# Optimization experiments

Measured on AMD Instinct MI355X. Metric: run time of the kernel, lower is better.

The kernel has to match this reference:

```python
import jax, jax.numpy as jnp
import numpy as np

NUM_ENT = 10000
NUM_REL = 230
S_DIM = 96
T_DIM = 32
DIM = S_DIM + T_DIM  # 128
N = 32768   # neighbors
Q = 4096    # unique query entities
E = 32768   # pooling edges
B = 1024    # batch triples
BN_EPS = 1e-5


def setup_inputs() -> dict:
    key = jax.random.key(0)
    ks = jax.random.split(key, 32)
    inp = {}
    inp["neighbor_idx"] = jax.random.randint(ks[0], (N,), 0, NUM_ENT)
    inp["rel_id"] = jax.random.randint(ks[1], (N,), 0, 2 * NUM_REL)
    inp["years"] = jax.random.uniform(ks[2], (N, 1), jnp.float32)
    inp["months"] = jax.random.uniform(ks[3], (N, 1), jnp.float32)
    inp["days"] = jax.random.uniform(ks[4], (N, 1), jnp.float32)
    inp["pool_src"] = jax.random.randint(ks[5], (E,), 0, N)
    inp["pool_dst"] = jax.random.randint(ks[6], (E,), 0, Q)
    inp["head_pos"] = jax.random.randint(ks[7], (B,), 0, Q)
    inp["tail_pos"] = jax.random.randint(ks[8], (B,), 0, Q)
    inp["rels"] = jax.random.randint(ks[9], (B,), 0, NUM_REL)
    # parameters (xavier-ish scales)
    inp["ent_embs"] = jax.random.normal(ks[10], (NUM_ENT, S_DIM), jnp.float32) * 0.05
    names = ["y_freq", "y_phi", "y_amp", "m_freq", "m_phi", "m_amp", "d_freq", "d_phi", "d_amp"]
    for i, n in enumerate(names):
        inp[n] = jax.random.normal(ks[11 + i], (NUM_ENT, T_DIM), jnp.float32) * 0.05
    inp["rel_embs"] = jax.random.normal(ks[20], (NUM_REL, DIM), jnp.float32) * 0.05
    inp["W"] = jax.random.normal(ks[21], (2 * NUM_REL, DIM, DIM), jnp.float32) * (1.0 / np.sqrt(DIM))
    inp["b"] = jnp.zeros((2 * NUM_REL, DIM), jnp.float32)
    inp["gamma"] = jnp.ones((2 * NUM_REL, DIM), jnp.float32)
    inp["beta"] = jnp.zeros((2 * NUM_REL, DIM), jnp.float32)
    return inp


def _forward(ent_embs, y_freq, y_phi, y_amp, m_freq, m_phi, m_amp,
             d_freq, d_phi, d_amp, rel_embs, W, b, gamma, beta,
             years, months, days,
             neighbor_idx, rel_id, pool_src, pool_dst, head_pos, tail_pos, rels):
    # diachronic time embedding: amp * sin(freq * t + phi), summed over y/m/d
    ty = y_amp[neighbor_idx] * jnp.sin(y_freq[neighbor_idx] * years + y_phi[neighbor_idx])
    tm = m_amp[neighbor_idx] * jnp.sin(m_freq[neighbor_idx] * months + m_phi[neighbor_idx])
    td = d_amp[neighbor_idx] * jnp.sin(d_freq[neighbor_idx] * days + d_phi[neighbor_idx])
    x = jnp.concatenate([ent_embs[neighbor_idx], ty + tm + td], axis=1)  # [N, DIM]

    # per-relation Linear (gather weights per neighbor)
    z = jnp.einsum('nd,nde->ne', x, W[rel_id]) + b[rel_id]  # [N, DIM]

    # per-relation-bucket BatchNorm (training stats, biased var); skipped for singleton buckets
    R2 = 2 * NUM_REL
    cnt = jax.ops.segment_sum(jnp.ones((z.shape[0],), z.dtype), rel_id, num_segments=R2)
    denom = jnp.maximum(cnt, 1.0)[:, None]
    mean = jax.ops.segment_sum(z, rel_id, num_segments=R2) / denom
    var = jax.ops.segment_sum(z * z, rel_id, num_segments=R2) / denom - mean * mean
    var = jnp.maximum(var, 0.0)
    zn = (z - mean[rel_id]) * jax.lax.rsqrt(var[rel_id] + BN_EPS) * gamma[rel_id] + beta[rel_id]
    z = jnp.where((cnt[rel_id] > 1.0)[:, None], zn, z)
    z = jax.nn.relu(z)

    # average pooling of neighbor features per query entity (PoolingLayer 'avg')
    psum = jax.ops.segment_sum(z[pool_src], pool_dst, num_segments=Q)
    pcnt = jax.ops.segment_sum(jnp.ones((pool_src.shape[0],), z.dtype), pool_dst, num_segments=Q)
    emb = psum / jnp.maximum(pcnt, 1.0)[:, None]  # [Q, DIM]

    # TransE-style scoring: -||h + r - t||_2 (dropout p=0 / eval mode)
    diff = emb[head_pos] + rel_embs[rels] - emb[tail_pos]
    return -jnp.sqrt(jnp.sum(diff * diff, axis=1))


def reference(neighbor_idx, rel_id, years, months, days, pool_src, pool_dst,
              head_pos, tail_pos, rels, ent_embs, y_freq, y_phi, y_amp,
              m_freq, m_phi, m_amp, d_freq, d_phi, d_amp, rel_embs, W, b, gamma, beta):
    return _forward(ent_embs, y_freq, y_phi, y_amp, m_freq, m_phi, m_amp,
                    d_freq, d_phi, d_amp, rel_embs, W, b, gamma, beta,
                    years, months, days,
                    neighbor_idx, rel_id, pool_src, pool_dst, head_pos, tail_pos, rels)
```

## Files before the change

### kernel.cpp

```cpp
#include <hip/hip_runtime.h>
#include <math.h>

#define NUM_ENT 10000
#define NUM_REL 230
#define R2      460
#define S_DIM   96
#define T_DIM   32
#define DIM     128
#define N_NBR   32768
#define Q_ENT   4096
#define E_EDGE  32768
#define B_TRI   1024
#define BN_EPS  1e-5f
#define CHUNK   64

typedef __attribute__((ext_vector_type(8))) short bf16x8;
typedef __attribute__((ext_vector_type(4))) float f32x4;

__device__ __forceinline__ unsigned short f2bf(float f) {
    unsigned int u = __float_as_uint(f);
    u = (u + 0x7FFFu + ((u >> 16) & 1u)) >> 16;
    return (unsigned short)u;
}
__device__ __forceinline__ float bf2f(unsigned short us) {
    return __uint_as_float((unsigned int)us << 16);
}

__device__ __forceinline__ int XIDX(int m, int d) {
    return (m * DIM + d) ^ ((m & 7) << 3);
}

__global__ void k_zero(int* __restrict__ p, int n4) {
    int i = blockIdx.x * blockDim.x + threadIdx.x;
    if (i < n4) ((int4*)p)[i] = make_int4(0, 0, 0, 0);
}

__global__ __launch_bounds__(256, 2) void k_front(
    const float* __restrict__ W, unsigned short* __restrict__ Wfrag,
    const int* __restrict__ rel, const int* __restrict__ pdst,
    int* __restrict__ hist_rel, int* __restrict__ hist_dst)
{
    const int t = threadIdx.x;
    if (blockIdx.x >= R2) {
        const int i = (blockIdx.x - R2) * 256 + t;
        if (i < N_NBR) atomicAdd(&hist_rel[rel[i]], 1);
        if (i < E_EDGE) atomicAdd(&hist_dst[pdst[i]], 1);
        return;
    }
    const int r = blockIdx.x;
    __shared__ float Wl[DIM * DIM];
    {
        const float4* Wg = (const float4*)(W + (size_t)r * DIM * DIM);
        float4* Wl4 = (float4*)Wl;
        #pragma unroll
        for (int i = 0; i < 16; ++i)
            Wl4[t + i * 256] = Wg[t + i * 256];
    }
    __syncthreads();
    unsigned short* dst = Wfrag + (size_t)r * DIM * DIM;
    #pragma unroll
    for (int it = 0; it < 8; ++it) {
        const int id = t + it * 256;
        const int lane = id & 63;
        const int h    = (id >> 6) & 1;
        const int wv   = (id >> 7) & 3;
        const int kk   = (id >> 9) & 3;
        const int n  = 32 * wv + 16 * h + (lane & 15);
        const int kb = 32 * kk + 8 * (lane >> 4);
        ushort4 lo, hi;
        lo.x = f2bf(Wl[(kb + 0) * DIM + n]);
        lo.y = f2bf(Wl[(kb + 1) * DIM + n]);
        lo.z = f2bf(Wl[(kb + 2) * DIM + n]);
        lo.w = f2bf(Wl[(kb + 3) * DIM + n]);
        hi.x = f2bf(Wl[(kb + 4) * DIM + n]);
        hi.y = f2bf(Wl[(kb + 5) * DIM + n]);
        hi.z = f2bf(Wl[(kb + 6) * DIM + n]);
        hi.w = f2bf(Wl[(kb + 7) * DIM + n]);
        *(ushort4*)&dst[id * 8]     = lo;
        *(ushort4*)&dst[id * 8 + 4] = hi;
    }
}

__global__ void k_scan_both(const int* __restrict__ hist_rel, int* __restrict__ offsets,
                            int* __restrict__ cur_rel,
                            const int* __restrict__ hist_dst, int* __restrict__ dst_off,
                            int* __restrict__ cur_dst)
{
    __shared__ int s[1024];
    const int t = threadIdx.x;
    if (blockIdx.x == 0) {
        const int h = (t < R2) ? hist_rel[t] : 0;
        if (t < 512) s[t] = h;
        __syncthreads();
        for (int off = 1; off < 512; off <<= 1) {
            int a = (t >= off && t < 512) ? s[t - off] : 0;
            __syncthreads();
            if (t < 512) s[t] += a;
            __syncthreads();
        }
        if (t == 0) offsets[0] = 0;
        if (t < R2) {
            offsets[t + 1] = s[t];
            cur_rel[t] = s[t] - h;
        }
    } else {
        const int base = t * 4;
        int v0 = hist_dst[base], v1 = hist_dst[base + 1];
        int v2 = hist_dst[base + 2], v3 = hist_dst[base + 3];
        s[t] = v0 + v1 + v2 + v3;
        __syncthreads();
        for (int off = 1; off < 1024; off <<= 1) {
            int a = (t >= off) ? s[t - off] : 0;
            __syncthreads();
            s[t] += a;
            __syncthreads();
        }
        int run = (t > 0) ? s[t - 1] : 0;
        dst_off[base] = run; cur_dst[base] = run; run += v0;
        dst_off[base + 1] = run; cur_dst[base + 1] = run; run += v1;
        dst_off[base + 2] = run; cur_dst[base + 2] = run; run += v2;
        dst_off[base + 3] = run; cur_dst[base + 3] = run; run += v3;
        if (t == 1023) dst_off[4096] = run;
    }
}

__global__ void k_scatter(const int* __restrict__ rel,
                          int* __restrict__ cur_rel, int* __restrict__ order,
                          int* __restrict__ rankpack,
                          const int* __restrict__ psrc, const int* __restrict__ pdst,
                          int* __restrict__ cur_dst, int* __restrict__ eorder_src) {
    int i = blockIdx.x * blockDim.x + threadIdx.x;
    if (i < N_NBR) {
        const int r = rel[i];
        const int pos = atomicAdd(&cur_rel[r], 1);
        order[pos] = i;
        rankpack[i] = pos | (r << 17);
    }
    if (i < E_EDGE) {
        eorder_src[atomicAdd(&cur_dst[pdst[i]], 1)] = psrc[i];
    }
}

__global__ __launch_bounds__(512, 4) void k_matvec(
    const int* __restrict__ order, const int* __restrict__ offsets,
    const int* __restrict__ nbr,
    const float* __restrict__ years, const float* __restrict__ months, const float* __restrict__ days,
    const float* __restrict__ ent,
    const float* __restrict__ yf, const float* __restrict__ yp, const float* __restrict__ ya,
    const float* __restrict__ mf, const float* __restrict__ mp, const float* __restrict__ ma,
    const float* __restrict__ df, const float* __restrict__ dp, const float* __restrict__ da,
    const unsigned short* __restrict__ Wfrag, const float* __restrict__ bias,
    const float* __restrict__ gamma, const float* __restrict__ beta,
    unsigned short* __restrict__ z_s, float2* __restrict__ scsh)
{
    const int r     = blockIdx.x;
    const int start = offsets[r];
    const int cnt   = offsets[r + 1] - start;

    __shared__ __align__(16) unsigned short Xl[2][CHUNK * DIM];
    __shared__ int s_ord[2][CHUNK];
    __shared__ int s_ni[2][CHUNK];
    __shared__ float bnred[8][2][16][2];

    const int t    = threadIdx.x;
    const int wid  = t >> 6;
    const int half = wid >> 2;
    const int wv   = wid & 3;
    const int lane = t & 63;
    const int l15  = lane & 15;
    const int g    = lane >> 4;

    const int nn0 = 32 * wv + l15;
    const int nn1 = nn0 + 16;
    const float bv0 = bias[r * DIM + nn0];
    const float bv1 = bias[r * DIM + nn1];

    float lsum0 = 0.f, lsq0 = 0.f, lsum1 = 0.f, lsq1 = 0.f;
    const unsigned short* Wr = Wfrag + (size_t)r * DIM * DIM;

    for (int cbase = 0; cbase < cnt; cbase += 2 * CHUNK) {
        const int hbase = cbase + half * CHUNK;
        const int mcnt  = min(CHUNK, max(0, cnt - hbase));

        if (t < 2 * CHUNK) {
            const int hh = t >> 6;
            const int m  = t & 63;
            const int gb = cbase + hh * CHUNK;
            int o = -1, ni = 0;
            if (gb + m < cnt) { o = order[start + gb + m]; ni = nbr[o]; }
            s_ord[hh][m] = o;
            s_ni[hh][m]  = ni;
        }
        __syncthreads();

        if (mcnt > 0) {
            const int lt = t & 255;
            const int m = lt >> 2, s = lt & 3;
            const int ni = s_ni[half][m];
            const bool vm = (m < mcnt);
            #pragma unroll
            for (int kk = 0; kk < 6; ++kk) {
                const int d = 4 * (s + 4 * kk);
                float4 e = *(const float4*)(ent + (size_t)ni * S_DIM + d);
                ushort4 b;
                b.x = vm ? f2bf(e.x) : 0; b.y = vm ? f2bf(e.y) : 0;
                b.z = vm ? f2bf(e.z) : 0; b.w = vm ? f2bf(e.w) : 0;
                *(ushort4*)&Xl[half][XIDX(m, d)] = b;
            }
            const int o = s_ord[half][m] < 0 ? 0 : s_ord[half][m];
            const float yr = years[o], mo = months[o], dy = days[o];
            #pragma unroll
            for (int hh = 0; hh < 2; ++hh) {
                const int j0 = s * 8 + hh * 4;
                const size_t tb = (size_t)ni * T_DIM + j0;
                const float4 vyf = *(const float4*)(yf + tb), vyp = *(const float4*)(yp + tb), vya = *(const float4*)(ya + tb);
                const float4 vmf = *(const float4*)(mf + tb), vmp = *(const float4*)(mp + tb), vma = *(const float4*)(ma + tb);
                const float4 vdf = *(const float4*)(df + tb), vdp = *(const float4*)(dp + tb), vda = *(const float4*)(da + tb);
                ushort4 b;
                #pragma unroll
                for (int j = 0; j < 4; ++j) {
                    const float fy = ((const float*)&vyf)[j] * yr + ((const float*)&vyp)[j];
                    const float fm = ((const float*)&vmf)[j] * mo + ((const float*)&vmp)[j];
                    const float fd = ((const float*)&vdf)[j] * dy + ((const float*)&vdp)[j];
                    float v = ((const float*)&vya)[j] * sinf(fy)
                            + ((const float*)&vma)[j] * sinf(fm)
                            + ((const float*)&vda)[j] * sinf(fd);
                    ((unsigned short*)&b)[j] = vm ? f2bf(v) : 0;
                }
                *(ushort4*)&Xl[half][XIDX(m, S_DIM + j0)] = b;
            }
        }
        __syncthreads();

        if (mcnt > 0) {
            f32x4 acc[4][2];
            #pragma unroll
            for (int i = 0; i < 4; ++i)
                #pragma unroll
                for (int j = 0; j < 2; ++j) acc[i][j] = (f32x4)0.f;

            #pragma unroll
            for (int kk = 0; kk < 4; ++kk) {
                const int k0 = kk * 32;
                bf16x8 a[4];
                #pragma unroll
                for (int mt = 0; mt < 4; ++mt)
                    a[mt] = *(const bf16x8*)&Xl[half][XIDX(16 * mt + l15, k0 + 8 * g)];
                const bf16x8 b0 = *(const bf16x8*)&Wr[(size_t)((kk * 4 + wv) * 2 + 0) * 512 + lane * 8];
                const bf16x8 b1 = *(const bf16x8*)&Wr[(size_t)((kk * 4 + wv) * 2 + 1) * 512 + lane * 8];
                #pragma unroll
                for (int mt = 0; mt < 4; ++mt) {
                    acc[mt][0] = __builtin_amdgcn_mfma_f32_16x16x32_bf16(a[mt], b0, acc[mt][0], 0, 0, 0);
                    acc[mt][1] = __builtin_amdgcn_mfma_f32_16x16x32_bf16(a[mt], b1, acc[mt][1], 0, 0, 0);
                }
            }

            #pragma unroll
            for (int mt = 0; mt < 4; ++mt) {
                #pragma unroll
                for (int reg = 0; reg < 4; ++reg) {
                    const int ml = 16 * mt + 4 * g + reg;
                    if (ml < mcnt) {
                        const float v0 = acc[mt][0][reg] + bv0;
                        const float v1 = acc[mt][1][reg] + bv1;
                        const size_t row = (size_t)(start + hbase + ml) * DIM;
                        z_s[row + nn0] = f2bf(v0);
                        z_s[row + nn1] = f2bf(v1);
                        lsum0 += v0; lsq0 += v0 * v0;
                        lsum1 += v1; lsq1 += v1 * v1;
                    }
                }
            }
        }
        __syncthreads();
    }

    lsum0 += __shfl_xor(lsum0, 16); lsum0 += __shfl_xor(lsum0, 32);
    lsq0  += __shfl_xor(lsq0, 16);  lsq0  += __shfl_xor(lsq0, 32);
    lsum1 += __shfl_xor(lsum1, 16); lsum1 += __shfl_xor(lsum1, 32);
    lsq1  += __shfl_xor(lsq1, 16);  lsq1  += __shfl_xor(lsq1, 32);
    if (g == 0) {
        bnred[wid][0][l15][0] = lsum0; bnred[wid][0][l15][1] = lsq0;
        bnred[wid][1][l15][0] = lsum1; bnred[wid][1][l15][1] = lsq1;
    }
    __syncthreads();
    if (half == 0 && g == 0) {
        #pragma unroll
        for (int nt = 0; nt < 2; ++nt) {
            const int col = 32 * wv + 16 * nt + l15;
            const float s = bnred[wid][nt][l15][0] + bnred[wid + 4][nt][l15][0];
            const float q = bnred[wid][nt][l15][1] + bnred[wid + 4][nt][l15][1];
            float sc = 1.f, sh = 0.f;
            if (cnt > 1) {
                const float mean = s / (float)cnt;
                const float var  = fmaxf(q / (float)cnt - mean * mean, 0.f);
                const int gi = r * DIM + col;
                sc = gamma[gi] * rsqrtf(var + BN_EPS);
                sh = beta[gi] - mean * sc;
            }
            scsh[r * DIM + col] = make_float2(sc, sh);
        }
    }
}

__global__ void k_pool2(const int* __restrict__ eorder_src, const int* __restrict__ dst_off,
                        const int* __restrict__ rankpack,
                        const unsigned short* __restrict__ z_s,
                        const float2* __restrict__ scsh,
                        float* __restrict__ emb)
{
    const int q = blockIdx.x;
    const int d = threadIdx.x;
    const int e0 = dst_off[q], e1 = dst_off[q + 1];
    float acc = 0.f;
    for (int e = e0; e < e1; ++e) {
        const int pk = rankpack[eorder_src[e]];
        const int p  = pk & 0x1FFFF;
        const int r  = pk >> 17;
        const float2 ss = scsh[r * DIM + d];
        const float v = bf2f(z_s[(size_t)p * DIM + d]) * ss.x + ss.y;
        acc += fmaxf(v, 0.f);
    }
    emb[(size_t)q * DIM + d] = (e1 > e0) ? acc / (float)(e1 - e0) : 0.f;
}

__global__ void k_score(const int* __restrict__ head, const int* __restrict__ tail,
                        const int* __restrict__ rels,
                        const float* __restrict__ emb, const float* __restrict__ rel_embs,
                        float* __restrict__ out)
{
    const int b = blockIdx.x;
    const int d = threadIdx.x;
    const int h = head[b], tq = tail[b], r = rels[b];

    const float diff = emb[(size_t)h * DIM + d] + rel_embs[r * DIM + d]
                     - emb[(size_t)tq * DIM + d];
    float sq = diff * diff;
    for (int off = 32; off > 0; off >>= 1) sq += __shfl_down(sq, off);
    __shared__ float partial[2];
    if ((threadIdx.x & 63) == 0) partial[threadIdx.x >> 6] = sq;
    __syncthreads();
    if (threadIdx.x == 0) out[b] = -sqrtf(partial[0] + partial[1]);
}

extern "C" void kernel_launch(void* const* d_in, const int* in_sizes, int n_in,
                              void* d_out, int out_size, void* d_ws, size_t ws_size,
                              hipStream_t stream) {
    const int*   neighbor_idx = (const int*)  d_in[0];
    const int*   rel_id       = (const int*)  d_in[1];
    const float* years        = (const float*)d_in[2];
    const float* months       = (const float*)d_in[3];
    const float* days         = (const float*)d_in[4];
    const int*   pool_src     = (const int*)  d_in[5];
    const int*   pool_dst     = (const int*)  d_in[6];
    const int*   head_pos     = (const int*)  d_in[7];
    const int*   tail_pos     = (const int*)  d_in[8];
    const int*   rels         = (const int*)  d_in[9];
    const float* ent_embs     = (const float*)d_in[10];
    const float* y_freq       = (const float*)d_in[11];
    const float* y_phi        = (const float*)d_in[12];
    const float* y_amp        = (const float*)d_in[13];
    const float* m_freq       = (const float*)d_in[14];
    const float* m_phi        = (const float*)d_in[15];
    const float* m_amp        = (const float*)d_in[16];
    const float* d_freq       = (const float*)d_in[17];
    const float* d_phi        = (const float*)d_in[18];
    const float* d_amp        = (const float*)d_in[19];
    const float* rel_embs     = (const float*)d_in[20];
    const float* W            = (const float*)d_in[21];
    const float* bias         = (const float*)d_in[22];
    const float* gamma        = (const float*)d_in[23];
    const float* beta         = (const float*)d_in[24];

    float* out = (float*)d_out;

    float* ws = (float*)d_ws;
    size_t off = 0;
    unsigned short* Wfrag = (unsigned short*)(ws + off); off += (size_t)R2 * DIM * DIM / 2;
    unsigned short* z_s   = (unsigned short*)(ws + off); off += (size_t)N_NBR * DIM / 2;
    float* emb   = ws + off; off += (size_t)Q_ENT * DIM;
    float2* scsh = (float2*)(ws + off); off += (size_t)R2 * DIM * 2;
    int* hist_rel = (int*)(ws + off); off += R2;
    int* hist_dst = (int*)(ws + off); off += Q_ENT;
    int* offsets  = (int*)(ws + off); off += R2 + 1;
    int* cur_rel  = (int*)(ws + off); off += R2;
    int* dst_off  = (int*)(ws + off); off += Q_ENT + 1;
    int* cur_dst  = (int*)(ws + off); off += Q_ENT;
    int* order    = (int*)(ws + off); off += N_NBR;
    int* rankpack = (int*)(ws + off); off += N_NBR;
    int* eorder_src = (int*)(ws + off); off += E_EDGE;

    const int nzero4 = (R2 + Q_ENT + 3) / 4;
    k_zero<<<(nzero4 + 255) / 256, 256, 0, stream>>>(hist_rel, nzero4);

    k_front<<<R2 + (N_NBR + 255) / 256, 256, 0, stream>>>(
        W, Wfrag, rel_id, pool_dst, hist_rel, hist_dst);

    k_scan_both<<<2, 1024, 0, stream>>>(hist_rel, offsets, cur_rel,
                                        hist_dst, dst_off, cur_dst);

    k_scatter<<<(N_NBR + 255) / 256, 256, 0, stream>>>(rel_id, cur_rel, order, rankpack,
                                                       pool_src, pool_dst, cur_dst, eorder_src);

    k_matvec<<<R2, 512, 0, stream>>>(order, offsets, neighbor_idx,
                                     years, months, days, ent_embs,
                                     y_freq, y_phi, y_amp,
                                     m_freq, m_phi, m_amp,
                                     d_freq, d_phi, d_amp,
                                     Wfrag, bias, gamma, beta,
                                     z_s, scsh);

    k_pool2<<<Q_ENT, DIM, 0, stream>>>(eorder_src, dst_off, rankpack,
                                       z_s, scsh, emb);

    k_score<<<B_TRI, DIM, 0, stream>>>(head_pos, tail_pos, rels, emb, rel_embs, out);
}
```

Baseline: 75.78 us.

## Fuse pooling into matvec via relation-grouped edges and atomic accumulation

Pooling edges are now grouped by the relation of their source neighbor instead of by destination. Each matvec block applies BN and ReLU and scatter-adds its rows into psum with float atomics, which removes the separate pool kernel and the scale/shift buffer. The histogram pass records atomic tickets, so the scan and scatter merge into one placement kernel where every block redundantly scans the small relation histograms. The cost is heavy atomic traffic on psum, a larger zeroing pass, nondeterministic summation order, and a packing limit of 15 bits for the source index.

```diff
diff --git a/kernel.cpp b/kernel.cpp
--- a/kernel.cpp
+++ b/kernel.cpp
@@ -37,14 +37,21 @@
 
 __global__ __launch_bounds__(256, 2) void k_front(
     const float* __restrict__ W, unsigned short* __restrict__ Wfrag,
-    const int* __restrict__ rel, const int* __restrict__ pdst,
-    int* __restrict__ hist_rel, int* __restrict__ hist_dst)
+    const int* __restrict__ rel, const int* __restrict__ psrc,
+    const int* __restrict__ pdst,
+    int* __restrict__ hist_rel, int* __restrict__ histE,
+    int* __restrict__ pcnt,
+    int* __restrict__ ticket_n, int* __restrict__ ticket_e)
 {
     const int t = threadIdx.x;
     if (blockIdx.x >= R2) {
         const int i = (blockIdx.x - R2) * 256 + t;
-        if (i < N_NBR) atomicAdd(&hist_rel[rel[i]], 1);
-        if (i < E_EDGE) atomicAdd(&hist_dst[pdst[i]], 1);
+        if (i < N_NBR) ticket_n[i] = atomicAdd(&hist_rel[rel[i]], 1);
+        if (i < E_EDGE) {
+            const int s = psrc[i];
+            ticket_e[i] = atomicAdd(&histE[rel[s]], 1);
+            atomicAdd(&pcnt[pdst[i]], 1);
+        }
         return;
     }
     const int r = blockIdx.x;
@@ -81,68 +88,83 @@
     }
 }
 
-__global__ void k_scan_both(const int* __restrict__ hist_rel, int* __restrict__ offsets,
-                            int* __restrict__ cur_rel,
-                            const int* __restrict__ hist_dst, int* __restrict__ dst_off,
-                            int* __restrict__ cur_dst)
+__global__ __launch_bounds__(256) void k_place(
+    const int* __restrict__ rel, const int* __restrict__ psrc,
+    const int* __restrict__ pdst,
+    const int* __restrict__ hist_rel, const int* __restrict__ histE,
+    const int* __restrict__ ticket_n, const int* __restrict__ ticket_e,
+    int* __restrict__ offsets, int* __restrict__ eoff,
+    int* __restrict__ order, int* __restrict__ rankpack,
+    int* __restrict__ epack)
 {
-    __shared__ int s[1024];
+    __shared__ int hA[512], hB[512], part[256];
     const int t = threadIdx.x;
-    if (blockIdx.x == 0) {
-        const int h = (t < R2) ? hist_rel[t] : 0;
-        if (t < 512) s[t] = h;
-        __syncthreads();
-        for (int off = 1; off < 512; off <<= 1) {
-            int a = (t >= off && t < 512) ? s[t - off] : 0;
-            __syncthreads();
-            if (t < 512) s[t] += a;
-            __syncthreads();
-        }
-        if (t == 0) offsets[0] = 0;
-        if (t < R2) {
-            offsets[t + 1] = s[t];
-            cur_rel[t] = s[t] - h;
-        }
-    } else {
-        const int base = t * 4;
-        int v0 = hist_dst[base], v1 = hist_dst[base + 1];
-        int v2 = hist_dst[base + 2], v3 = hist_dst[base + 3];
-        s[t] = v0 + v1 + v2 + v3;
-        __syncthreads();
-        for (int off = 1; off < 1024; off <<= 1) {
-            int a = (t >= off) ? s[t - off] : 0;
-            __syncthreads();
-            s[t] += a;
-            __syncthreads();
-        }
-        int run = (t > 0) ? s[t - 1] : 0;
-        dst_off[base] = run; cur_dst[base] = run; run += v0;
-        dst_off[base + 1] = run; cur_dst[base + 1] = run; run += v1;
-        dst_off[base + 2] = run; cur_dst[base + 2] = run; run += v2;
-        dst_off[base + 3] = run; cur_dst[base + 3] = run; run += v3;
-        if (t == 1023) dst_off[4096] = run;
-    }
-}
-
-__global__ void k_scatter(const int* __restrict__ rel,
-                          int* __restrict__ cur_rel, int* __restrict__ order,
-                          int* __restrict__ rankpack,
-                          const int* __restrict__ psrc, const int* __restrict__ pdst,
-                          int* __restrict__ cur_dst, int* __restrict__ eorder_src) {
-    int i = blockIdx.x * blockDim.x + threadIdx.x;
+    const int b = blockIdx.x;
+    hA[t]       = (t < R2) ? hist_rel[t] : 0;
+    hA[t + 256] = (t + 256 < R2) ? hist_rel[t + 256] : 0;
+    hB[t]       = (t < R2) ? histE[t] : 0;
+    hB[t + 256] = (t + 256 < R2) ? histE[t + 256] : 0;
+    __syncthreads();
+
+    const int a0 = hA[2 * t], a1 = hA[2 * t + 1];
+    part[t] = a0 + a1;
+    __syncthreads();
+    for (int off = 1; off < 256; off <<= 1) {
+        int v = (t >= off) ? part[t - off] : 0;
+        __syncthreads();
+        part[t] += v;
+        __syncthreads();
+    }
+    {
+        const int ex = t ? part[t - 1] : 0;
+        hA[2 * t] = ex; hA[2 * t + 1] = ex + a0;
+        if (b == 0) {
+            if (2 * t < R2)     offsets[2 * t]     = ex;
+            if (2 * t + 1 < R2) offsets[2 * t + 1] = ex + a0;
+            if (t == 255)       offsets[R2]        = part[255];
+        }
+    }
+    __syncthreads();
+
+    const int b0 = hB[2 * t], b1 = hB[2 * t + 1];
+    part[t] = b0 + b1;
+    __syncthreads();
+    for (int off = 1; off < 256; off <<= 1) {
+        int v = (t >= off) ? part[t - off] : 0;
+        __syncthreads();
+        part[t] += v;
+        __syncthreads();
+    }
+    {
+        const int ex = t ? part[t - 1] : 0;
+        hB[2 * t] = ex; hB[2 * t + 1] = ex + b0;
+        if (b == 0) {
+            if (2 * t < R2)     eoff[2 * t]     = ex;
+            if (2 * t + 1 < R2) eoff[2 * t + 1] = ex + b0;
+            if (t == 255)       eoff[R2]        = part[255];
+        }
+    }
+    __syncthreads();
+
+    const int i = b * 256 + t;
     if (i < N_NBR) {
         const int r = rel[i];
-        const int pos = atomicAdd(&cur_rel[r], 1);
+        const int pos = hA[r] + ticket_n[i];
         order[pos] = i;
-        rankpack[i] = pos | (r << 17);
+        rankpack[i] = pos;
     }
     if (i < E_EDGE) {
-        eorder_src[atomicAdd(&cur_dst[pdst[i]], 1)] = psrc[i];
+        const int s = psrc[i];
+        const int kr = rel[s];
+        const int epos = hB[kr] + ticket_e[i];
+        epack[epos] = s | (pdst[i] << 15);
     }
 }
 
 __global__ __launch_bounds__(512, 4) void k_matvec(
     const int* __restrict__ order, const int* __restrict__ offsets,
+    const int* __restrict__ eoff, const int* __restrict__ epack,
+    const int* __restrict__ rankpack,
     const int* __restrict__ nbr,
     const float* __restrict__ years, const float* __restrict__ months, const float* __restrict__ days,
     const float* __restrict__ ent,
@@ -151,7 +173,7 @@
     const float* __restrict__ df, const float* __restrict__ dp, const float* __restrict__ da,
     const unsigned short* __restrict__ Wfrag, const float* __restrict__ bias,
     const float* __restrict__ gamma, const float* __restrict__ beta,
-    unsigned short* __restrict__ z_s, float2* __restrict__ scsh)
+    unsigned short* __restrict__ z_s, float* __restrict__ psum)
 {
     const int r     = blockIdx.x;
     const int start = offsets[r];
@@ -161,6 +183,7 @@
     __shared__ int s_ord[2][CHUNK];
     __shared__ int s_ni[2][CHUNK];
     __shared__ float bnred[8][2][16][2];
+    __shared__ float scl[DIM], shf[DIM];
 
     const int t    = threadIdx.x;
     const int wid  = t >> 6;
@@ -298,43 +321,41 @@
                 sc = gamma[gi] * rsqrtf(var + BN_EPS);
                 sh = beta[gi] - mean * sc;
             }
-            scsh[r * DIM + col] = make_float2(sc, sh);
-        }
-    }
-}
-
-__global__ void k_pool2(const int* __restrict__ eorder_src, const int* __restrict__ dst_off,
-                        const int* __restrict__ rankpack,
-                        const unsigned short* __restrict__ z_s,
-                        const float2* __restrict__ scsh,
-                        float* __restrict__ emb)
-{
-    const int q = blockIdx.x;
-    const int d = threadIdx.x;
-    const int e0 = dst_off[q], e1 = dst_off[q + 1];
-    float acc = 0.f;
-    for (int e = e0; e < e1; ++e) {
-        const int pk = rankpack[eorder_src[e]];
-        const int p  = pk & 0x1FFFF;
-        const int r  = pk >> 17;
-        const float2 ss = scsh[r * DIM + d];
-        const float v = bf2f(z_s[(size_t)p * DIM + d]) * ss.x + ss.y;
-        acc += fmaxf(v, 0.f);
-    }
-    emb[(size_t)q * DIM + d] = (e1 > e0) ? acc / (float)(e1 - e0) : 0.f;
+            scl[col] = sc;
+            shf[col] = sh;
+        }
+    }
+    __syncthreads();
+
+    {
+        const int e0 = eoff[r], e1 = eoff[r + 1];
+        const int grp = t >> 7;
+        const int d   = t & 127;
+        const float psc = scl[d], psh = shf[d];
+        for (int e = e0 + grp; e < e1; e += 4) {
+            const int pk  = epack[e];
+            const int s   = pk & 0x7FFF;
+            const int q   = pk >> 15;
+            const int row = rankpack[s];
+            const float v = fmaxf(bf2f(z_s[(size_t)row * DIM + d]) * psc + psh, 0.f);
+            atomicAdd(&psum[(size_t)q * DIM + d], v);
+        }
+    }
 }
 
 __global__ void k_score(const int* __restrict__ head, const int* __restrict__ tail,
                         const int* __restrict__ rels,
-                        const float* __restrict__ emb, const float* __restrict__ rel_embs,
+                        const float* __restrict__ psum, const int* __restrict__ pcnt,
+                        const float* __restrict__ rel_embs,
                         float* __restrict__ out)
 {
     const int b = blockIdx.x;
     const int d = threadIdx.x;
     const int h = head[b], tq = tail[b], r = rels[b];
 
-    const float diff = emb[(size_t)h * DIM + d] + rel_embs[r * DIM + d]
-                     - emb[(size_t)tq * DIM + d];
+    const float eh = psum[(size_t)h  * DIM + d] / fmaxf((float)pcnt[h],  1.f);
+    const float et = psum[(size_t)tq * DIM + d] / fmaxf((float)pcnt[tq], 1.f);
+    const float diff = eh + rel_embs[r * DIM + d] - et;
     float sq = diff * diff;
     for (int off = 32; off > 0; off >>= 1) sq += __shfl_down(sq, off);
     __shared__ float partial[2];
@@ -378,40 +399,39 @@
     size_t off = 0;
     unsigned short* Wfrag = (unsigned short*)(ws + off); off += (size_t)R2 * DIM * DIM / 2;
     unsigned short* z_s   = (unsigned short*)(ws + off); off += (size_t)N_NBR * DIM / 2;
-    float* emb   = ws + off; off += (size_t)Q_ENT * DIM;
-    float2* scsh = (float2*)(ws + off); off += (size_t)R2 * DIM * 2;
+    float* psum   = ws + off; off += (size_t)Q_ENT * DIM;
+    int* pcnt     = (int*)(ws + off); off += Q_ENT;
     int* hist_rel = (int*)(ws + off); off += R2;
-    int* hist_dst = (int*)(ws + off); off += Q_ENT;
+    int* histE    = (int*)(ws + off); off += R2;
+    int* ticket_n = (int*)(ws + off); off += N_NBR;
+    int* ticket_e = (int*)(ws + off); off += E_EDGE;
     int* offsets  = (int*)(ws + off); off += R2 + 1;
-    int* cur_rel  = (int*)(ws + off); off += R2;
-    int* dst_off  = (int*)(ws + off); off += Q_ENT + 1;
-    int* cur_dst  = (int*)(ws + off); off += Q_ENT;
+    int* eoff     = (int*)(ws + off); off += R2 + 1;
     int* order    = (int*)(ws + off); off += N_NBR;
     int* rankpack = (int*)(ws + off); off += N_NBR;
-    int* eorder_src = (int*)(ws + off); off += E_EDGE;
-
-    const int nzero4 = (R2 + Q_ENT + 3) / 4;
-    k_zero<<<(nzero4 + 255) / 256, 256, 0, stream>>>(hist_rel, nzero4);
+    int* epack    = (int*)(ws + off); off += E_EDGE;
+
+    const int nzero  = Q_ENT * DIM + Q_ENT + 2 * R2;
+    const int nzero4 = nzero / 4;
+    k_zero<<<(nzero4 + 255) / 256, 256, 0, stream>>>((int*)psum, nzero4);
 
     k_front<<<R2 + (N_NBR + 255) / 256, 256, 0, stream>>>(
-        W, Wfrag, rel_id, pool_dst, hist_rel, hist_dst);
-
-    k_scan_both<<<2, 1024, 0, stream>>>(hist_rel, offsets, cur_rel,
-                                        hist_dst, dst_off, cur_dst);
-
-    k_scatter<<<(N_NBR + 255) / 256, 256, 0, stream>>>(rel_id, cur_rel, order, rankpack,
-                                                       pool_src, pool_dst, cur_dst, eorder_src);
-
-    k_matvec<<<R2, 512, 0, stream>>>(order, offsets, neighbor_idx,
+        W, Wfrag, rel_id, pool_src, pool_dst,
+        hist_rel, histE, pcnt, ticket_n, ticket_e);
+
+    k_place<<<(N_NBR + 255) / 256, 256, 0, stream>>>(
+        rel_id, pool_src, pool_dst, hist_rel, histE,
+        ticket_n, ticket_e, offsets, eoff, order, rankpack, epack);
+
+    k_matvec<<<R2, 512, 0, stream>>>(order, offsets, eoff, epack, rankpack,
+                                     neighbor_idx,
                                      years, months, days, ent_embs,
                                      y_freq, y_phi, y_amp,
                                      m_freq, m_phi, m_amp,
                                      d_freq, d_phi, d_amp,
                                      Wfrag, bias, gamma, beta,
-                                     z_s, scsh);
-
-    k_pool2<<<Q_ENT, DIM, 0, stream>>>(eorder_src, dst_off, rankpack,
-                                       z_s, scsh, emb);
-
-    k_score<<<B_TRI, DIM, 0, stream>>>(head_pos, tail_pos, rels, emb, rel_embs, out);
-}
+                                     z_s, psum);
+
+    k_score<<<B_TRI, DIM, 0, stream>>>(head_pos, tail_pos, rels,
+                                       psum, pcnt, rel_embs, out);
+}
```

After: 79.55 us. +5.0%, slower.
